# Optimization experiments

Measured on AMD Instinct MI355X. Metric: run time of the kernel, lower is better.

## Reference

```python
import jax, jax.numpy as jnp
import numpy as np

VOCAB = 50000
EMB = 512
HID = 512
OUT = 2
B = 64
T = 512

def setup_inputs() -> dict:
    key = jax.random.key(0)
    k1, k2, k3, k4, k5, k6 = jax.random.split(key, 6)
    x = jax.random.randint(k1, (B, T), 0, VOCAB, dtype=jnp.int32)
    emb = jax.random.normal(k2, (VOCAB, EMB), dtype=jnp.float32) * 0.02
    emb = emb.at[0].set(0.0)  # padding_idx row zeroed
    W1 = jax.random.normal(k3, (HID, 2 * EMB), dtype=jnp.float32) * (1.0 / np.sqrt(2 * EMB))
    b1 = jax.random.normal(k4, (HID,), dtype=jnp.float32) * 0.01
    W2 = jax.random.normal(k5, (OUT, HID), dtype=jnp.float32) * (1.0 / np.sqrt(HID))
    b2 = jax.random.normal(k6, (OUT,), dtype=jnp.float32) * 0.01
    return {"x": x, "emb": emb, "W1": W1, "b1": b1, "W2": W2, "b2": b2}

def reference(x, emb, W1, b1, W2, b2):
    xe = emb[x]                      # [B, T, E]
    h0 = jnp.zeros((x.shape[0], emb.shape[1]), dtype=emb.dtype)

    def step(h, xt):                 # xt: [B, E], h: [B, H]
        inp = jnp.concatenate([xt, h], axis=1)        # [B, 2E]
        h_new = jnp.tanh(inp @ W1.T + b1)             # [B, H]
        return h_new, h_new

    hT, outs = jax.lax.scan(step, h0, jnp.swapaxes(xe, 0, 1))  # outs: [T, B, H]
    pooled = jnp.max(outs, axis=0)                    # max over time -> [B, H]
    logits = pooled @ W2.T + b2                       # [B, OUT]
    return logits, hT
```

## Files before the change

### kernel.cpp

```cpp
#include <hip/hip_runtime.h>
#include <math.h>

#define TT   512
#define BB   64
#define EMBD 512
#define HIDD 512

typedef _Float16 half2v __attribute__((ext_vector_type(2)));
typedef _Float16 half8  __attribute__((ext_vector_type(8)));
typedef float    f32x4  __attribute__((ext_vector_type(4)));

__device__ __forceinline__ float fdot2(unsigned a, unsigned b, float c) {
  half2v av = __builtin_bit_cast(half2v, a);
  half2v bv = __builtin_bit_cast(half2v, b);
  return __builtin_amdgcn_fdot2(av, bv, c, false);
}

__device__ __forceinline__ float fast_tanh(float x) {
  float e = __expf(2.0f * x);
  return 1.0f - 2.0f * __builtin_amdgcn_rcpf(e + 1.0f);
}

__device__ __forceinline__ unsigned pack2(float a, float b) {
  half2v hv; hv.x = (_Float16)a; hv.y = (_Float16)b;
  return __builtin_bit_cast(unsigned, hv);
}

__device__ __forceinline__ uint4 pack8(float4 f0, float4 f1) {
  uint4 u;
  u.x = pack2(f0.x, f0.y); u.y = pack2(f0.z, f0.w);
  u.z = pack2(f1.x, f1.y); u.w = pack2(f1.z, f1.w);
  return u;
}

__global__ __launch_bounds__(256) void repack_w1h(
    const float* __restrict__ W1, uint4* __restrict__ wp)
{
  const int gid = blockIdx.x * 256 + threadIdx.x;
  const int c   = gid >> 9;
  const int tid = gid & 511;
  const int w = tid >> 6, l = tid & 63;
  const int q = w & 3, hh = w >> 2;
  const int jo = c & 3, kq = c >> 2;
  const int j  = 256 * hh + 4 * l + jo;
  const int k0 = 128 * q + 8 * kq;
  const float* src = W1 + (size_t)j * (2 * EMBD) + EMBD + k0;
  unsigned r[4];
#pragma unroll
  for (int p = 0; p < 4; p++) r[p] = pack2(src[2 * p], src[2 * p + 1]);
  uint4 u; u.x = r[0]; u.y = r[1]; u.z = r[2]; u.w = r[3];
  wp[gid] = u;
}

__global__ __launch_bounds__(256, 1) void px_mfma(
    const int* __restrict__ xx, const float* __restrict__ emb,
    const float* __restrict__ W1, const float* __restrict__ b1,
    float* __restrict__ px)
{
  __shared__ uint4 At[128 * 16];
  __shared__ uint4 Bt[256 * 16];
  __shared__ int stok[128];

  const int tid = threadIdx.x;
  const int wv  = tid >> 6, l = tid & 63;
  const int m0  = blockIdx.x * 128;
  const int j0  = blockIdx.y * 256;

  if (tid < 128) stok[tid] = xx[m0 + tid];

  f32x4 acc[8][4];
#pragma unroll
  for (int q = 0; q < 4; q++) {
    const float bc = b1[j0 + wv * 64 + 16 * q + (l & 15)];
#pragma unroll
    for (int i = 0; i < 8; i++) { acc[i][q].x = bc; acc[i][q].y = bc; acc[i][q].z = bc; acc[i][q].w = bc; }
  }

  for (int kc = 0; kc < 4; kc++) {
    __syncthreads();
    {
      const int r = tid >> 1, h = tid & 1;
      const float4* s4 = (const float4*)(emb + (size_t)stok[r] * EMBD + kc * 128 + h * 64);
#pragma unroll
      for (int i = 0; i < 8; i++)
        At[r * 16 + ((8 * h + i) ^ (r & 15))] = pack8(s4[2 * i], s4[2 * i + 1]);
      const float4* t4 = (const float4*)(W1 + (size_t)(j0 + tid) * (2 * EMBD) + kc * 128);
#pragma unroll
      for (int i = 0; i < 16; i++)
        Bt[tid * 16 + (i ^ (tid & 15))] = pack8(t4[2 * i], t4[2 * i + 1]);
    }
    __syncthreads();

#pragma unroll
    for (int ks = 0; ks < 4; ks++) {
      const int so = ks * 4 + (l >> 4);
      half8 a[8], bfr[4];
#pragma unroll
      for (int i = 0; i < 8; i++) {
        const int ra = 16 * i + (l & 15);
        a[i] = __builtin_bit_cast(half8, At[ra * 16 + (so ^ (ra & 15))]);
      }
#pragma unroll
      for (int q = 0; q < 4; q++) {
        const int rb = wv * 64 + 16 * q + (l & 15);
        bfr[q] = __builtin_bit_cast(half8, Bt[rb * 16 + (so ^ (rb & 15))]);
      }
#pragma unroll
      for (int i = 0; i < 8; i++)
#pragma unroll
        for (int q = 0; q < 4; q++)
          acc[i][q] = __builtin_amdgcn_mfma_f32_16x16x32_f16(a[i], bfr[q], acc[i][q], 0, 0, 0);
    }
  }

#pragma unroll
  for (int i = 0; i < 8; i++) {
    const int mrow = m0 + 16 * i + (l >> 4) * 4;
#pragma unroll
    for (int q = 0; q < 4; q++) {
      const int col = j0 + wv * 64 + 16 * q + (l & 15);
      float* dst = px + (size_t)mrow * HIDD + col;
      dst[0 * HIDD] = acc[i][q].x;
      dst[1 * HIDD] = acc[i][q].y;
      dst[2 * HIDD] = acc[i][q].z;
      dst[3 * HIDD] = acc[i][q].w;
    }
  }
}

#define DOT4(HH, W0, W1v, W2v, W3v) do {                                    \
    const uint4 hh = (HH);                                                  \
    a0=fdot2((W0).x,hh.x,a0);  a0=fdot2((W0).y,hh.y,a0);                    \
    a0=fdot2((W0).z,hh.z,a0);  a0=fdot2((W0).w,hh.w,a0);                    \
    a1=fdot2((W1v).x,hh.x,a1); a1=fdot2((W1v).y,hh.y,a1);                   \
    a1=fdot2((W1v).z,hh.z,a1); a1=fdot2((W1v).w,hh.w,a1);                   \
    a2=fdot2((W2v).x,hh.x,a2); a2=fdot2((W2v).y,hh.y,a2);                   \
    a2=fdot2((W2v).z,hh.z,a2); a2=fdot2((W2v).w,hh.w,a2);                   \
    a3=fdot2((W3v).x,hh.x,a3); a3=fdot2((W3v).y,hh.y,a3);                   \
    a3=fdot2((W3v).z,hh.z,a3); a3=fdot2((W3v).w,hh.w,a3);                   \
  } while (0)

__attribute__((amdgpu_flat_work_group_size(512, 512),
               amdgpu_waves_per_eu(2), amdgpu_num_vgpr(256)))
__global__ void elman_v12(
    const uint4* __restrict__ wp, const float* __restrict__ px,
    const float* __restrict__ W2, const float* __restrict__ b2,
    float* __restrict__ out)
{
  __shared__ uint4 wlds[15 * 512];
  __shared__ __align__(16) unsigned short hbuf[HIDD];
  __shared__ float parts[4][HIDD];
  __shared__ float red[2][8];

  const int b   = blockIdx.x;
  const int tid = threadIdx.x;
  const int w   = tid >> 6, l = tid & 63;
  const int q   = w & 3;
  const int hh  = w >> 2;
  const int jb  = 256 * hh + 4 * l;

  uint4 wr[49];
#pragma unroll
  for (int i = 0; i < 49; i++) wr[i] = wp[(size_t)i * 512 + tid];
#pragma unroll
  for (int i = 0; i < 15; i++) wlds[i * 512 + tid] = wp[(size_t)(49 + i) * 512 + tid];
  if (tid < 64) ((uint4*)hbuf)[tid] = make_uint4(0u, 0u, 0u, 0u);
  __syncthreads();

  const uint4* hq = (const uint4*)hbuf + 16 * q;
  const float* pxj = px + (size_t)b * TT * HIDD + tid;
  float rmq = -INFINITY;

  for (int t = 0; t < TT; t++) {
    float pxs = pxj[(size_t)t * HIDD];
    const uint4 p0 = wlds[11 * 512 + tid];
    const uint4 p1 = wlds[12 * 512 + tid];
    const uint4 p2 = wlds[13 * 512 + tid];
    const uint4 p3 = wlds[14 * 512 + tid];

    float a0 = 0.f, a1 = 0.f, a2 = 0.f, a3 = 0.f;

#pragma unroll
    for (int kq = 0; kq < 12; kq++)
      DOT4(hq[kq], wr[4 * kq + 0], wr[4 * kq + 1], wr[4 * kq + 2], wr[4 * kq + 3]);
    DOT4(hq[12], wr[48],
         wlds[0 * 512 + tid], wlds[1 * 512 + tid], wlds[2 * 512 + tid]);
    DOT4(hq[13], wlds[3 * 512 + tid], wlds[4 * 512 + tid],
         wlds[5 * 512 + tid], wlds[6 * 512 + tid]);
    DOT4(hq[14], wlds[7 * 512 + tid], wlds[8 * 512 + tid],
         wlds[9 * 512 + tid], wlds[10 * 512 + tid]);
    DOT4(hq[15], p0, p1, p2, p3);

    *(float4*)&parts[q][jb] = make_float4(a0, a1, a2, a3);
    __syncthreads();

    float s = parts[0][tid] + parts[1][tid] + parts[2][tid] + parts[3][tid] + pxs;
    float hv = fast_tanh(s);
    rmq = fmaxf(rmq, hv);
    _Float16 hf = (_Float16)hv;
    hbuf[tid] = __builtin_bit_cast(unsigned short, hf);
    if (t == TT - 1)
      out[2 * BB + (size_t)b * HIDD + tid] = hv;
    __syncthreads();
  }

  {
    float q0 = rmq * W2[tid];
    float q1 = rmq * W2[HIDD + tid];
#pragma unroll
    for (int off = 32; off; off >>= 1) {
      q0 += __shfl_down(q0, off);
      q1 += __shfl_down(q1, off);
    }
    if (l == 0) { red[0][w] = q0; red[1][w] = q1; }
  }
  __syncthreads();
  if (tid < 2) {
    float s = b2[tid];
#pragma unroll
    for (int i = 0; i < 8; i++) s += red[tid][i];
    out[b * 2 + tid] = s;
  }
}

extern "C" void kernel_launch(void* const* d_in, const int* in_sizes, int n_in,
                              void* d_out, int out_size, void* d_ws, size_t ws_size,
                              hipStream_t stream)
{
  const int*   x   = (const int*)d_in[0];
  const float* emb = (const float*)d_in[1];
  const float* W1  = (const float*)d_in[2];
  const float* b1  = (const float*)d_in[3];
  const float* W2  = (const float*)d_in[4];
  const float* b2  = (const float*)d_in[5];
  float* out = (float*)d_out;
  char* ws = (char*)d_ws;

  uint4* wp = (uint4*)ws;
  float* px = (float*)(ws + (1 << 19));
  const size_t need = (size_t)(1 << 19) + (size_t)BB * TT * HIDD * sizeof(float);
  if (ws_size < need) return;

  repack_w1h<<<128, 256, 0, stream>>>(W1, wp);
  px_mfma<<<dim3(TT * BB / 128, HIDD / 256), 256, 0, stream>>>(x, emb, W1, b1, px);
  elman_v12<<<dim3(BB), dim3(512), 0, stream>>>(wp, px, W2, b2, out);
}
```

Before: 762.9 us.

## Drop one barrier per step via double-buffered partials and per-wave h slices

The recurrent kernel now double-buffers the cross-wave partial-sum array. Each wave redundantly finishes the tanh for the 128 hidden units it consumes in the next step, writing them into its own private slice of the h buffer. Because each wave only reads h values it produced itself, the second __syncthreads per timestep is removed. The cost is duplicated reduction and tanh work across the two wave halves, plus slightly more shared memory.

```diff
diff --git a/kernel.cpp b/kernel.cpp
--- a/kernel.cpp
+++ b/kernel.cpp
@@ -129,27 +129,27 @@
 }
 
 #define DOT4(HH, W0, W1v, W2v, W3v) do {                                    \
-    const uint4 hh = (HH);                                                  \
-    a0=fdot2((W0).x,hh.x,a0);  a0=fdot2((W0).y,hh.y,a0);                    \
-    a0=fdot2((W0).z,hh.z,a0);  a0=fdot2((W0).w,hh.w,a0);                    \
-    a1=fdot2((W1v).x,hh.x,a1); a1=fdot2((W1v).y,hh.y,a1);                   \
-    a1=fdot2((W1v).z,hh.z,a1); a1=fdot2((W1v).w,hh.w,a1);                   \
-    a2=fdot2((W2v).x,hh.x,a2); a2=fdot2((W2v).y,hh.y,a2);                   \
-    a2=fdot2((W2v).z,hh.z,a2); a2=fdot2((W2v).w,hh.w,a2);                   \
-    a3=fdot2((W3v).x,hh.x,a3); a3=fdot2((W3v).y,hh.y,a3);                   \
-    a3=fdot2((W3v).z,hh.z,a3); a3=fdot2((W3v).w,hh.w,a3);                   \
+    const uint4 hh_ = (HH);                                                 \
+    a0=fdot2((W0).x,hh_.x,a0);  a0=fdot2((W0).y,hh_.y,a0);                  \
+    a0=fdot2((W0).z,hh_.z,a0);  a0=fdot2((W0).w,hh_.w,a0);                  \
+    a1=fdot2((W1v).x,hh_.x,a1); a1=fdot2((W1v).y,hh_.y,a1);                 \
+    a1=fdot2((W1v).z,hh_.z,a1); a1=fdot2((W1v).w,hh_.w,a1);                 \
+    a2=fdot2((W2v).x,hh_.x,a2); a2=fdot2((W2v).y,hh_.y,a2);                 \
+    a2=fdot2((W2v).z,hh_.z,a2); a2=fdot2((W2v).w,hh_.w,a2);                 \
+    a3=fdot2((W3v).x,hh_.x,a3); a3=fdot2((W3v).y,hh_.y,a3);                 \
+    a3=fdot2((W3v).z,hh_.z,a3); a3=fdot2((W3v).w,hh_.w,a3);                 \
   } while (0)
 
 __attribute__((amdgpu_flat_work_group_size(512, 512),
                amdgpu_waves_per_eu(2), amdgpu_num_vgpr(256)))
-__global__ void elman_v12(
+__global__ void elman_v13(
     const uint4* __restrict__ wp, const float* __restrict__ px,
     const float* __restrict__ W2, const float* __restrict__ b2,
     float* __restrict__ out)
 {
   __shared__ uint4 wlds[15 * 512];
-  __shared__ __align__(16) unsigned short hbuf[HIDD];
-  __shared__ float parts[4][HIDD];
+  __shared__ __align__(16) unsigned hbuf[8 * 64];
+  __shared__ float parts[2][4][HIDD];
   __shared__ float red[2][8];
 
   const int b   = blockIdx.x;
@@ -158,21 +158,24 @@
   const int q   = w & 3;
   const int hh  = w >> 2;
   const int jb  = 256 * hh + 4 * l;
+  const int jq  = 128 * q + 2 * l;
 
   uint4 wr[49];
 #pragma unroll
   for (int i = 0; i < 49; i++) wr[i] = wp[(size_t)i * 512 + tid];
 #pragma unroll
   for (int i = 0; i < 15; i++) wlds[i * 512 + tid] = wp[(size_t)(49 + i) * 512 + tid];
-  if (tid < 64) ((uint4*)hbuf)[tid] = make_uint4(0u, 0u, 0u, 0u);
-  __syncthreads();
-
-  const uint4* hq = (const uint4*)hbuf + 16 * q;
-  const float* pxj = px + (size_t)b * TT * HIDD + tid;
-  float rmq = -INFINITY;
+  if (tid < 128) ((uint4*)hbuf)[tid] = make_uint4(0u, 0u, 0u, 0u);
+  __syncthreads();
+
+  const uint4* hq  = (const uint4*)hbuf + w * 16;
+  const float* pxj = px + (size_t)b * TT * HIDD + jq;
+  float rm0 = -INFINITY, rm1 = -INFINITY;
 
   for (int t = 0; t < TT; t++) {
-    float pxs = pxj[(size_t)t * HIDD];
+    const int cur = t & 1;
+
+    const float2 pxv = *(const float2*)(pxj + (size_t)t * HIDD);
     const uint4 p0 = wlds[11 * 512 + tid];
     const uint4 p1 = wlds[12 * 512 + tid];
     const uint4 p2 = wlds[13 * 512 + tid];
@@ -191,22 +194,30 @@
          wlds[9 * 512 + tid], wlds[10 * 512 + tid]);
     DOT4(hq[15], p0, p1, p2, p3);
 
-    *(float4*)&parts[q][jb] = make_float4(a0, a1, a2, a3);
+    *(float4*)&parts[cur][q][jb] = make_float4(a0, a1, a2, a3);
     __syncthreads();
 
-    float s = parts[0][tid] + parts[1][tid] + parts[2][tid] + parts[3][tid] + pxs;
-    float hv = fast_tanh(s);
-    rmq = fmaxf(rmq, hv);
-    _Float16 hf = (_Float16)hv;
-    hbuf[tid] = __builtin_bit_cast(unsigned short, hf);
-    if (t == TT - 1)
-      out[2 * BB + (size_t)b * HIDD + tid] = hv;
-    __syncthreads();
-  }
-
+    const float2 s0 = *(const float2*)&parts[cur][0][jq];
+    const float2 s1 = *(const float2*)&parts[cur][1][jq];
+    const float2 s2 = *(const float2*)&parts[cur][2][jq];
+    const float2 s3 = *(const float2*)&parts[cur][3][jq];
+    const float h0 = fast_tanh(s0.x + s1.x + s2.x + s3.x + pxv.x);
+    const float h1 = fast_tanh(s0.y + s1.y + s2.y + s3.y + pxv.y);
+    rm0 = fmaxf(rm0, h0);
+    rm1 = fmaxf(rm1, h1);
+    hbuf[w * 64 + l] = pack2(h0, h1);
+    if (t == TT - 1 && hh == 0)
+      *(float2*)(out + 2 * BB + (size_t)b * HIDD + jq) = make_float2(h0, h1);
+  }
+
+  float* pl = (float*)parts;
+  __syncthreads();
+  if (hh == 0) *(float2*)&pl[jq] = make_float2(rm0, rm1);
+  __syncthreads();
   {
-    float q0 = rmq * W2[tid];
-    float q1 = rmq * W2[HIDD + tid];
+    float pv = pl[tid];
+    float q0 = pv * W2[tid];
+    float q1 = pv * W2[HIDD + tid];
 #pragma unroll
     for (int off = 32; off; off >>= 1) {
       q0 += __shfl_down(q0, off);
@@ -243,5 +254,5 @@
 
   repack_w1h<<<128, 256, 0, stream>>>(W1, wp);
   px_mfma<<<dim3(TT * BB / 128, HIDD / 256), 256, 0, stream>>>(x, emb, W1, b1, px);
-  elman_v12<<<dim3(BB), dim3(512), 0, stream>>>(wp, px, W2, b2, out);
-}
+  elman_v13<<<dim3(BB), dim3(512), 0, stream>>>(wp, px, W2, b2, out);
+}
```

Measured after the change: 764.5 us. About the same (+0.2%).
